# Kernel optimization log

Hardware: AMD Instinct MI355X
Metric: run time of the kernel (lower is better)

The kernel has to match this reference:

```python
import jax, jax.numpy as jnp
import numpy as np

N_NODES = 100000
N_EDGES = 1600000
D_IN, D_HID, D_OUT = 256, 256, 128


def setup_inputs() -> dict:
    key = jax.random.key(0)
    k1, k2, k3, k4, k5, k6 = jax.random.split(key, 6)
    x = jax.random.normal(k1, (N_NODES, D_IN), dtype=jnp.float32)
    edge_index = jax.random.randint(k2, (2, N_EDGES), 0, N_NODES, dtype=jnp.int64)
    W1 = jax.random.normal(k3, (D_IN, D_HID), dtype=jnp.float32) / np.sqrt(D_IN)
    b1 = jax.random.normal(k4, (D_HID,), dtype=jnp.float32) * 0.01
    W2 = jax.random.normal(k5, (D_HID, D_OUT), dtype=jnp.float32) / np.sqrt(D_HID)
    b2 = jax.random.normal(k6, (D_OUT,), dtype=jnp.float32) * 0.01
    return {"x": x, "edge_index": edge_index, "W1": W1, "b1": b1, "W2": W2, "b2": b2}


def _gcn_conv(x, src, dst, W, b, n_nodes):
    # PyG GCNConv: linear transform, add self-loops, symmetric normalization,
    # scatter-add aggregation, bias.
    h = x @ W                                         # [N, D_out]
    # degree including self-loop (edge weight 1)
    deg = jax.ops.segment_sum(jnp.ones((src.shape[0],), h.dtype), dst,
                              num_segments=n_nodes) + 1.0
    dinv = jax.lax.rsqrt(deg)                         # [N]
    norm = dinv[src] * dinv[dst]                      # [E]
    msg = h[src] * norm[:, None]                      # [E, D_out] gather + scale
    agg = jax.ops.segment_sum(msg, dst, num_segments=n_nodes)
    # self-loop contribution: norm_ii = dinv_i^2
    agg = agg + h * (dinv * dinv)[:, None]
    return agg + b


def reference(x, edge_index, W1, b1, W2, b2):
    src, dst = edge_index[0], edge_index[1]
    n = x.shape[0]
    h = _gcn_conv(x, src, dst, W1, b1, n)
    h = jax.nn.relu(h)
    out = _gcn_conv(h, src, dst, W2, b2, n)
    return out
```

## Files before the change

kernel.cpp:

```cpp
#include <hip/hip_runtime.h>

#define N_NODES 100000
#define N_EDGES 1600000
#define D_IN 256
#define D_HID 256
#define D_OUT 128
#define SLOTS 64

#define NB 1024
#define NPB 98
#define CAP 2048
#define BIN_T 8192

typedef unsigned int u32;
typedef unsigned short u16;
typedef __attribute__((ext_vector_type(8))) short bf16x8;
typedef __attribute__((ext_vector_type(8))) unsigned short u16x8;
typedef __attribute__((ext_vector_type(4))) float f32x4;

__device__ __forceinline__ u16 f2bf(float v) {
    u32 u = __float_as_uint(v);
    u32 r = (u + 0x7fffu + ((u >> 16) & 1u)) >> 16;
    return (u16)r;
}
__device__ __forceinline__ float bf2f(u16 b) {
    return __uint_as_float(((u32)b) << 16);
}

__global__ __launch_bounds__(256) void bin_kernel(const int* __restrict__ src,
                                                  const int* __restrict__ dst,
                                                  int* __restrict__ gcnt,
                                                  int* __restrict__ binned, int E,
                                                  const float* __restrict__ W1,
                                                  u16* __restrict__ w1hi,
                                                  const float* __restrict__ W2,
                                                  u16* __restrict__ w2hi) {
    const int t = threadIdx.x;
    const int gtid = blockIdx.x * 256 + t;
    const int gstride = gridDim.x * 256;
    for (int i = gtid; i < D_IN * D_HID; i += gstride) {
        const int k = i / D_HID, n = i - k * D_HID;
        w1hi[(size_t)n * D_IN + k] = f2bf(W1[i]);
    }
    for (int i = gtid; i < D_HID * D_OUT; i += gstride) {
        const int k = i / D_OUT, n = i - k * D_OUT;
        w2hi[(size_t)n * D_HID + k] = f2bf(W2[i]);
    }

    __shared__ int hist[NB];
    __shared__ int cur[NB];
    const int base = blockIdx.x * BIN_T;
#pragma unroll
    for (int q = 0; q < NB / 256; ++q) hist[q * 256 + t] = 0;
    __syncthreads();
#pragma unroll 4
    for (int j = 0; j < BIN_T / 256; ++j) {
        const int e = base + j * 256 + t;
        if (e < E) atomicAdd(&hist[dst[e] / NPB], 1);
    }
    __syncthreads();
#pragma unroll
    for (int q = 0; q < NB / 256; ++q) {
        const int b = q * 256 + t;
        const int c = hist[b];
        cur[b] = c ? atomicAdd(&gcnt[b], c) : 0;
    }
    __syncthreads();
#pragma unroll 4
    for (int j = 0; j < BIN_T / 256; ++j) {
        const int e = base + j * 256 + t;
        if (e < E) {
            const int d = dst[e];
            const int b = d / NPB;
            const int ld = d - b * NPB;
            const int r = atomicAdd(&cur[b], 1);
            if (r < CAP) binned[(size_t)b * CAP + r] = (ld << 17) | src[e];
        }
    }
}

__global__ __launch_bounds__(256) void bucket_scatter(const int* __restrict__ gcnt,
                                                      const int* __restrict__ binned,
                                                      int* __restrict__ deg,
                                                      int* __restrict__ slot,
                                                      float* __restrict__ dinv) {
    __shared__ int degw[NPB];
    __shared__ int slotw[NPB * SLOTS];
    const int b = blockIdx.x;
    const int t = threadIdx.x;
    const int nbase = b * NPB;
    for (int i = t; i < NPB; i += 256) degw[i] = 0;
    __syncthreads();
    int cnt = gcnt[b];
    if (cnt > CAP) cnt = CAP;
    const int* ep = &binned[(size_t)b * CAP];
    for (int i = t; i < cnt; i += 256) {
        const int v = ep[i];
        const int ld = v >> 17;
        const int s = v & 0x1FFFF;
        const int pos = atomicAdd(&degw[ld], 1);
        if (pos < SLOTS) slotw[ld * SLOTS + pos] = s;
    }
    __syncthreads();
    const int lim = min(NPB, N_NODES - nbase);
    if (lim <= 0) return;
    for (int i = t; i < lim * SLOTS; i += 256)
        slot[(size_t)nbase * SLOTS + i] = slotw[i];
    for (int i = t; i < lim; i += 256) {
        const int dgv = degw[i];
        deg[nbase + i] = dgv;
        dinv[nbase + i] = rsqrtf((float)dgv + 1.0f);
    }
}

template <bool AF32>
__global__ __launch_bounds__(256) void gemm_tile(
    const void* __restrict__ Aptr, const u16* __restrict__ B,
    u16* __restrict__ Cb, int M, int N, int K) {
    constexpr int ABYTES = AF32 ? 16384 : 8192;
    __shared__ char lds[2][ABYTES + 8192];
    const int t = threadIdx.x;
    const int wave = t >> 6;
    const int lane = t & 63;
    const int wm = wave >> 1, wn = wave & 1;
    const int mBase = blockIdx.y * 128;
    const int nBase = blockIdx.x * 128;

    f32x4 acc[4][4];
#pragma unroll
    for (int i = 0; i < 4; ++i)
#pragma unroll
        for (int j = 0; j < 4; ++j) acc[i][j] = (f32x4){0.f, 0.f, 0.f, 0.f};

    const int lr = lane >> 3;
    const int lp = lane & 7;
    const int lc = lp ^ lr;
    const int lr4 = lane >> 2;
    const int lc4 = (lane & 3) ^ (lr4 & 3);

    auto STAGE = [&](int buf, int kt) {
        const int k0 = kt * 32;
        if (AF32) {
            const float* A = (const float*)Aptr;
            const int coff = k0 + lc * 4;
#pragma unroll
            for (int q = 0; q < 4; ++q) {
                const int row = wave * 32 + q * 8 + lr;
                int mg = mBase + row;
                if (mg > M - 1) mg = M - 1;
                const float* s = A + (size_t)mg * K + coff;
                char* d = &lds[buf][(wave * 32 + q * 8) * 128];
                __builtin_amdgcn_global_load_lds(
                    (const __attribute__((address_space(1))) u32*)s,
                    (__attribute__((address_space(3))) u32*)d, 16, 0, 0);
            }
        } else {
            const u16* A = (const u16*)Aptr;
            const int coff = k0 + lc4 * 8;
#pragma unroll
            for (int q = 0; q < 2; ++q) {
                const int row = wave * 32 + q * 16 + lr4;
                int mg = mBase + row;
                if (mg > M - 1) mg = M - 1;
                const u16* s = A + (size_t)mg * K + coff;
                char* d = &lds[buf][(wave * 32 + q * 16) * 64];
                __builtin_amdgcn_global_load_lds(
                    (const __attribute__((address_space(1))) u32*)s,
                    (__attribute__((address_space(3))) u32*)d, 16, 0, 0);
            }
        }
        {
            const int coff = k0 + lc4 * 8;
#pragma unroll
            for (int q = 0; q < 2; ++q) {
                const int row = wave * 32 + q * 16 + lr4;
                const int ng = nBase + row;
                const u16* s = B + (size_t)ng * K + coff;
                char* d = &lds[buf][ABYTES + (wave * 32 + q * 16) * 64];
                __builtin_amdgcn_global_load_lds(
                    (const __attribute__((address_space(1))) u32*)s,
                    (__attribute__((address_space(3))) u32*)d, 16, 0, 0);
            }
        }
    };

    auto COMPUTE = [&](int buf) {
        const char* pa = &lds[buf][0];
        const char* pb = &lds[buf][ABYTES];
        const int lm = lane & 15;
        const int c4 = lane >> 4;
        bf16x8 ah[4], bh[4];
#pragma unroll
        for (int i = 0; i < 4; ++i) {
            const int r = wm * 64 + i * 16 + lm;
            if (AF32) {
                const int s = r & 7;
                const f32x4 a0 = *(const f32x4*)(pa + r * 128 + ((2 * c4) ^ s) * 16);
                const f32x4 a1 = *(const f32x4*)(pa + r * 128 + ((2 * c4 + 1) ^ s) * 16);
                bf16x8 h;
#pragma unroll
                for (int j = 0; j < 4; ++j)
                    h[j] = (short)((__float_as_uint(a0[j]) + 0x8000u) >> 16);
#pragma unroll
                for (int j = 0; j < 4; ++j)
                    h[4 + j] = (short)((__float_as_uint(a1[j]) + 0x8000u) >> 16);
                ah[i] = h;
            } else {
                ah[i] = *(const bf16x8*)(pa + r * 64 + (c4 ^ (r & 3)) * 16);
            }
        }
#pragma unroll
        for (int j = 0; j < 4; ++j) {
            const int r = wn * 64 + j * 16 + lm;
            bh[j] = *(const bf16x8*)(pb + r * 64 + (c4 ^ (r & 3)) * 16);
        }
#pragma unroll
        for (int i = 0; i < 4; ++i)
#pragma unroll
            for (int j = 0; j < 4; ++j)
                acc[i][j] = __builtin_amdgcn_mfma_f32_16x16x32_bf16(ah[i], bh[j], acc[i][j], 0, 0, 0);
    };

    const int NT = K / 32;
    STAGE(0, 0);
#pragma unroll 1
    for (int kt = 0; kt < NT; ++kt) {
        __syncthreads();
        if (kt + 1 < NT) STAGE((kt + 1) & 1, kt + 1);
        COMPUTE(kt & 1);
        __syncthreads();
    }

    const int lm = lane & 15;
    const int c4 = lane >> 4;
#pragma unroll
    for (int i = 0; i < 4; ++i) {
#pragma unroll
        for (int r = 0; r < 4; ++r) {
            const int row = mBase + wm * 64 + i * 16 + c4 * 4 + r;
            if (row < M) {
#pragma unroll
                for (int j = 0; j < 4; ++j) {
                    const int col = nBase + wn * 64 + j * 16 + lm;
                    Cb[(size_t)row * N + col] = f2bf(acc[i][j][r]);
                }
            }
        }
    }
}

__global__ __launch_bounds__(256) void gather_agg_bf16(const u16* __restrict__ h,
                                                       const int* __restrict__ deg,
                                                       const int* __restrict__ slot,
                                                       const float* __restrict__ dinv,
                                                       const float* __restrict__ bias,
                                                       u16* __restrict__ ob, int n) {
    const int node = blockIdx.x * 8 + (threadIdx.x >> 5);
    const int lane = threadIdx.x & 31;
    if (node >= n) return;
    const float di = dinv[node];
    int dg = deg[node];
    if (dg > SLOTS) dg = SLOTS;
    const int* sp = &slot[(size_t)node * SLOTS];
    const int off = lane * 8;

    float acc[8];
#pragma unroll
    for (int j = 0; j < 8; ++j) acc[j] = 0.f;

    int k = 0;
    for (; k + 1 < dg; k += 2) {
        const int s0 = sp[k];
        const int s1 = sp[k + 1];
        const float n0 = dinv[s0] * di;
        const float n1 = dinv[s1] * di;
        const u16x8 va = *(const u16x8*)&h[(size_t)s0 * 256 + off];
        const u16x8 vb = *(const u16x8*)&h[(size_t)s1 * 256 + off];
#pragma unroll
        for (int j = 0; j < 8; ++j)
            acc[j] += bf2f(va[j]) * n0 + bf2f(vb[j]) * n1;
    }
    if (k < dg) {
        const int s0 = sp[k];
        const float n0 = dinv[s0] * di;
        const u16x8 va = *(const u16x8*)&h[(size_t)s0 * 256 + off];
#pragma unroll
        for (int j = 0; j < 8; ++j) acc[j] += bf2f(va[j]) * n0;
    }

    const float sl = di * di;
    const u16x8 hv = *(const u16x8*)&h[(size_t)node * 256 + off];
    const float4 bv0 = *(const float4*)&bias[off];
    const float4 bv1 = *(const float4*)&bias[off + 4];
    const float bb[8] = {bv0.x, bv0.y, bv0.z, bv0.w, bv1.x, bv1.y, bv1.z, bv1.w};
    u16x8 H;
#pragma unroll
    for (int j = 0; j < 8; ++j)
        H[j] = f2bf(fmaxf(acc[j] + bf2f(hv[j]) * sl + bb[j], 0.f));
    *(u16x8*)&ob[(size_t)node * 256 + off] = H;
}

__global__ __launch_bounds__(256) void gather_agg_out(const u16* __restrict__ h,
                                                      const int* __restrict__ deg,
                                                      const int* __restrict__ slot,
                                                      const float* __restrict__ dinv,
                                                      const float* __restrict__ bias,
                                                      float* __restrict__ outp, int n) {
    const int node = blockIdx.x * 16 + (threadIdx.x >> 4);
    const int lane = threadIdx.x & 15;
    if (node >= n) return;
    const float di = dinv[node];
    int dg = deg[node];
    if (dg > SLOTS) dg = SLOTS;
    const int* sp = &slot[(size_t)node * SLOTS];
    const int off = lane * 8;

    float acc[8];
#pragma unroll
    for (int j = 0; j < 8; ++j) acc[j] = 0.f;

    int k = 0;
    for (; k + 1 < dg; k += 2) {
        const int s0 = sp[k];
        const int s1 = sp[k + 1];
        const float n0 = dinv[s0] * di;
        const float n1 = dinv[s1] * di;
        const u16x8 va = *(const u16x8*)&h[(size_t)s0 * 128 + off];
        const u16x8 vb = *(const u16x8*)&h[(size_t)s1 * 128 + off];
#pragma unroll
        for (int j = 0; j < 8; ++j)
            acc[j] += bf2f(va[j]) * n0 + bf2f(vb[j]) * n1;
    }
    if (k < dg) {
        const int s0 = sp[k];
        const float n0 = dinv[s0] * di;
        const u16x8 va = *(const u16x8*)&h[(size_t)s0 * 128 + off];
#pragma unroll
        for (int j = 0; j < 8; ++j) acc[j] += bf2f(va[j]) * n0;
    }

    const float sl = di * di;
    const u16x8 hv = *(const u16x8*)&h[(size_t)node * 128 + off];
    const float4 bv0 = *(const float4*)&bias[off];
    const float4 bv1 = *(const float4*)&bias[off + 4];
    const float bb[8] = {bv0.x, bv0.y, bv0.z, bv0.w, bv1.x, bv1.y, bv1.z, bv1.w};
    float o[8];
#pragma unroll
    for (int j = 0; j < 8; ++j) o[j] = acc[j] + bf2f(hv[j]) * sl + bb[j];
    float4 o0 = make_float4(o[0], o[1], o[2], o[3]);
    float4 o1 = make_float4(o[4], o[5], o[6], o[7]);
    *(float4*)&outp[(size_t)node * 128 + off] = o0;
    *(float4*)&outp[(size_t)node * 128 + off + 4] = o1;
}

extern "C" void kernel_launch(void* const* d_in, const int* in_sizes, int n_in,
                              void* d_out, int out_size, void* d_ws, size_t ws_size,
                              hipStream_t stream) {
    const float* x  = (const float*)d_in[0];
    const int*   ei = (const int*)d_in[1];
    const float* W1 = (const float*)d_in[2];
    const float* b1 = (const float*)d_in[3];
    const float* W2 = (const float*)d_in[4];
    const float* b2 = (const float*)d_in[5];
    float* out = (float*)d_out;

    const int* src = ei;
    const int* dst = ei + N_EDGES;

    char* ws = (char*)d_ws;
    float* dinv = (float*)(ws + 0x000000);
    int*   deg  = (int*)  (ws + 0x080000);
    int*   gcnt = (int*)  (ws + 0x100000);
    u16* wt1hi = (u16*)(ws + 0x200000);
    u16* wt2hi = (u16*)(ws + 0x240000);
    int* binned = (int*)(ws + 0x280000);
    int* slot   = (int*)(ws + 0xB00000);
    const size_t big = 0x2500000;
    u16* Phi = (u16*)(ws + big);
    u16* Hb  = (u16*)(ws + big + 51200000);

    hipMemsetAsync(gcnt, 0, NB * sizeof(int), stream);

    bin_kernel<<<(N_EDGES + BIN_T - 1) / BIN_T, 256, 0, stream>>>(
        src, dst, gcnt, binned, N_EDGES, W1, wt1hi, W2, wt2hi);
    bucket_scatter<<<NB, 256, 0, stream>>>(gcnt, binned, deg, slot, dinv);

    {
        dim3 g(D_HID / 128, (N_NODES + 127) / 128);
        gemm_tile<true><<<g, 256, 0, stream>>>(x, wt1hi, Hb, N_NODES, D_HID, D_IN);
    }
    gather_agg_bf16<<<(N_NODES + 7) / 8, 256, 0, stream>>>(
        Hb, deg, slot, dinv, b1, Phi, N_NODES);

    {
        dim3 g(D_OUT / 128, (N_NODES + 127) / 128);
        gemm_tile<false><<<g, 256, 0, stream>>>(Phi, wt2hi, Hb, N_NODES, D_OUT, D_HID);
    }
    gather_agg_out<<<(N_NODES + 15) / 16, 256, 0, stream>>>(
        Hb, deg, slot, dinv, b2, out, N_NODES);
}
```

Measured before the change: 325.7 us.

## Fuse edge binning with first GEMM in one launch, move weight conversion out

```diff
diff --git a/kernel.cpp b/kernel.cpp
--- a/kernel.cpp
+++ b/kernel.cpp
@@ -11,6 +11,9 @@
 #define NPB 98
 #define CAP 2048
 #define BIN_T 8192
+#define BIN_BLKS ((N_EDGES + BIN_T - 1) / BIN_T)
+#define GEMM1_ROWTILES ((N_NODES + 127) / 128)
+#define GEMM1_BLKS (GEMM1_ROWTILES * 2)
 
 typedef unsigned int u32;
 typedef unsigned short u16;
@@ -27,17 +30,13 @@
     return __uint_as_float(((u32)b) << 16);
 }
 
-__global__ __launch_bounds__(256) void bin_kernel(const int* __restrict__ src,
-                                                  const int* __restrict__ dst,
-                                                  int* __restrict__ gcnt,
-                                                  int* __restrict__ binned, int E,
-                                                  const float* __restrict__ W1,
-                                                  u16* __restrict__ w1hi,
-                                                  const float* __restrict__ W2,
-                                                  u16* __restrict__ w2hi) {
-    const int t = threadIdx.x;
-    const int gtid = blockIdx.x * 256 + t;
+__global__ __launch_bounds__(256) void weights_kernel(
+    const float* __restrict__ W1, u16* __restrict__ w1hi,
+    const float* __restrict__ W2, u16* __restrict__ w2hi,
+    int* __restrict__ gcnt) {
+    const int gtid = blockIdx.x * 256 + threadIdx.x;
     const int gstride = gridDim.x * 256;
+    for (int i = gtid; i < NB; i += gstride) gcnt[i] = 0;
     for (int i = gtid; i < D_IN * D_HID; i += gstride) {
         const int k = i / D_HID, n = i - k * D_HID;
         w1hi[(size_t)n * D_IN + k] = f2bf(W1[i]);
@@ -46,35 +45,161 @@
         const int k = i / D_OUT, n = i - k * D_OUT;
         w2hi[(size_t)n * D_HID + k] = f2bf(W2[i]);
     }
-
-    __shared__ int hist[NB];
-    __shared__ int cur[NB];
-    const int base = blockIdx.x * BIN_T;
-#pragma unroll
-    for (int q = 0; q < NB / 256; ++q) hist[q * 256 + t] = 0;
-    __syncthreads();
+}
+
+__global__ __launch_bounds__(256) void fused_bin_gemm1(
+    const int* __restrict__ src, const int* __restrict__ dst,
+    int* __restrict__ gcnt, int* __restrict__ binned,
+    const float* __restrict__ x, const u16* __restrict__ B,
+    u16* __restrict__ Cb) {
+    __shared__ char smem[49152];
+    const int t = threadIdx.x;
+
+    if (blockIdx.x < BIN_BLKS) {
+        int* hist = (int*)smem;
+        int* cur = hist + NB;
+        const int base = blockIdx.x * BIN_T;
+#pragma unroll
+        for (int q = 0; q < NB / 256; ++q) hist[q * 256 + t] = 0;
+        __syncthreads();
 #pragma unroll 4
-    for (int j = 0; j < BIN_T / 256; ++j) {
-        const int e = base + j * 256 + t;
-        if (e < E) atomicAdd(&hist[dst[e] / NPB], 1);
-    }
-    __syncthreads();
-#pragma unroll
-    for (int q = 0; q < NB / 256; ++q) {
-        const int b = q * 256 + t;
-        const int c = hist[b];
-        cur[b] = c ? atomicAdd(&gcnt[b], c) : 0;
-    }
-    __syncthreads();
+        for (int j = 0; j < BIN_T / 256; ++j) {
+            const int e = base + j * 256 + t;
+            if (e < N_EDGES) atomicAdd(&hist[dst[e] / NPB], 1);
+        }
+        __syncthreads();
+#pragma unroll
+        for (int q = 0; q < NB / 256; ++q) {
+            const int b = q * 256 + t;
+            const int c = hist[b];
+            cur[b] = c ? atomicAdd(&gcnt[b], c) : 0;
+        }
+        __syncthreads();
 #pragma unroll 4
-    for (int j = 0; j < BIN_T / 256; ++j) {
-        const int e = base + j * 256 + t;
-        if (e < E) {
-            const int d = dst[e];
-            const int b = d / NPB;
-            const int ld = d - b * NPB;
-            const int r = atomicAdd(&cur[b], 1);
-            if (r < CAP) binned[(size_t)b * CAP + r] = (ld << 17) | src[e];
+        for (int j = 0; j < BIN_T / 256; ++j) {
+            const int e = base + j * 256 + t;
+            if (e < N_EDGES) {
+                const int d = dst[e];
+                const int b = d / NPB;
+                const int ld = d - b * NPB;
+                const int r = atomicAdd(&cur[b], 1);
+                if (r < CAP) binned[(size_t)b * CAP + r] = (ld << 17) | src[e];
+            }
+        }
+        return;
+    }
+
+    const int bid = blockIdx.x - BIN_BLKS;
+    const int mBase = (bid >> 1) * 128;
+    const int nBase = (bid & 1) * 128;
+    constexpr int ABYTES = 16384;
+    constexpr int BUF = ABYTES + 8192;
+    const int wave = t >> 6;
+    const int lane = t & 63;
+    const int wm = wave >> 1, wn = wave & 1;
+    const int K = D_IN, N = D_HID, M = N_NODES;
+
+    f32x4 acc[4][4];
+#pragma unroll
+    for (int i = 0; i < 4; ++i)
+#pragma unroll
+        for (int j = 0; j < 4; ++j) acc[i][j] = (f32x4){0.f, 0.f, 0.f, 0.f};
+
+    const int lr = lane >> 3;
+    const int lp = lane & 7;
+    const int lc = lp ^ lr;
+    const int lr4 = lane >> 2;
+    const int lc4 = (lane & 3) ^ (lr4 & 3);
+
+    auto STAGE = [&](int buf, int kt) {
+        const int k0 = kt * 32;
+        char* ldsbuf = smem + buf * BUF;
+        {
+            const int coff = k0 + lc * 4;
+#pragma unroll
+            for (int q = 0; q < 4; ++q) {
+                const int row = wave * 32 + q * 8 + lr;
+                int mg = mBase + row;
+                if (mg > M - 1) mg = M - 1;
+                const float* s = x + (size_t)mg * K + coff;
+                char* d = ldsbuf + (wave * 32 + q * 8) * 128;
+                __builtin_amdgcn_global_load_lds(
+                    (const __attribute__((address_space(1))) u32*)s,
+                    (__attribute__((address_space(3))) u32*)d, 16, 0, 0);
+            }
+        }
+        {
+            const int coff = k0 + lc4 * 8;
+#pragma unroll
+            for (int q = 0; q < 2; ++q) {
+                const int row = wave * 32 + q * 16 + lr4;
+                const int ng = nBase + row;
+                const u16* s = B + (size_t)ng * K + coff;
+                char* d = ldsbuf + ABYTES + (wave * 32 + q * 16) * 64;
+                __builtin_amdgcn_global_load_lds(
+                    (const __attribute__((address_space(1))) u32*)s,
+                    (__attribute__((address_space(3))) u32*)d, 16, 0, 0);
+            }
+        }
+    };
+
+    auto COMPUTE = [&](int buf) {
+        const char* pa = smem + buf * BUF;
+        const char* pb = pa + ABYTES;
+        const int lm = lane & 15;
+        const int c4 = lane >> 4;
+        bf16x8 ah[4], bh[4];
+#pragma unroll
+        for (int i = 0; i < 4; ++i) {
+            const int r = wm * 64 + i * 16 + lm;
+            const int s = r & 7;
+            const f32x4 a0 = *(const f32x4*)(pa + r * 128 + ((2 * c4) ^ s) * 16);
+            const f32x4 a1 = *(const f32x4*)(pa + r * 128 + ((2 * c4 + 1) ^ s) * 16);
+            bf16x8 h;
+#pragma unroll
+            for (int j = 0; j < 4; ++j)
+                h[j] = (short)((__float_as_uint(a0[j]) + 0x8000u) >> 16);
+#pragma unroll
+            for (int j = 0; j < 4; ++j)
+                h[4 + j] = (short)((__float_as_uint(a1[j]) + 0x8000u) >> 16);
+            ah[i] = h;
+        }
+#pragma unroll
+        for (int j = 0; j < 4; ++j) {
+            const int r = wn * 64 + j * 16 + lm;
+            bh[j] = *(const bf16x8*)(pb + r * 64 + (c4 ^ (r & 3)) * 16);
+        }
+#pragma unroll
+        for (int i = 0; i < 4; ++i)
+#pragma unroll
+            for (int j = 0; j < 4; ++j)
+                acc[i][j] = __builtin_amdgcn_mfma_f32_16x16x32_bf16(ah[i], bh[j], acc[i][j], 0, 0, 0);
+    };
+
+    const int NT = K / 32;
+    STAGE(0, 0);
+#pragma unroll 1
+    for (int kt = 0; kt < NT; ++kt) {
+        __syncthreads();
+        if (kt + 1 < NT) STAGE((kt + 1) & 1, kt + 1);
+        COMPUTE(kt & 1);
+        __syncthreads();
+    }
+
+    const int lm = lane & 15;
+    const int c4 = lane >> 4;
+#pragma unroll
+    for (int i = 0; i < 4; ++i) {
+#pragma unroll
+        for (int r = 0; r < 4; ++r) {
+            const int row = mBase + wm * 64 + i * 16 + c4 * 4 + r;
+            if (row < M) {
+#pragma unroll
+                for (int j = 0; j < 4; ++j) {
+                    const int col = nBase + wn * 64 + j * 16 + lm;
+                    Cb[(size_t)row * N + col] = f2bf(acc[i][j][r]);
+                }
+            }
         }
     }
 }
@@ -113,11 +238,10 @@
     }
 }
 
-template <bool AF32>
-__global__ __launch_bounds__(256) void gemm_tile(
-    const void* __restrict__ Aptr, const u16* __restrict__ B,
+__global__ __launch_bounds__(256) void gemm_bf16(
+    const u16* __restrict__ A, const u16* __restrict__ B,
     u16* __restrict__ Cb, int M, int N, int K) {
-    constexpr int ABYTES = AF32 ? 16384 : 8192;
+    constexpr int ABYTES = 8192;
     __shared__ char lds[2][ABYTES + 8192];
     const int t = threadIdx.x;
     const int wave = t >> 6;
@@ -132,55 +256,32 @@
 #pragma unroll
         for (int j = 0; j < 4; ++j) acc[i][j] = (f32x4){0.f, 0.f, 0.f, 0.f};
 
-    const int lr = lane >> 3;
-    const int lp = lane & 7;
-    const int lc = lp ^ lr;
     const int lr4 = lane >> 2;
     const int lc4 = (lane & 3) ^ (lr4 & 3);
 
     auto STAGE = [&](int buf, int kt) {
         const int k0 = kt * 32;
-        if (AF32) {
-            const float* A = (const float*)Aptr;
-            const int coff = k0 + lc * 4;
-#pragma unroll
-            for (int q = 0; q < 4; ++q) {
-                const int row = wave * 32 + q * 8 + lr;
-                int mg = mBase + row;
-                if (mg > M - 1) mg = M - 1;
-                const float* s = A + (size_t)mg * K + coff;
-                char* d = &lds[buf][(wave * 32 + q * 8) * 128];
-                __builtin_amdgcn_global_load_lds(
-                    (const __attribute__((address_space(1))) u32*)s,
-                    (__attribute__((address_space(3))) u32*)d, 16, 0, 0);
-            }
-        } else {
-            const u16* A = (const u16*)Aptr;
-            const int coff = k0 + lc4 * 8;
-#pragma unroll
-            for (int q = 0; q < 2; ++q) {
-                const int row = wave * 32 + q * 16 + lr4;
-                int mg = mBase + row;
-                if (mg > M - 1) mg = M - 1;
-                const u16* s = A + (size_t)mg * K + coff;
-                char* d = &lds[buf][(wave * 32 + q * 16) * 64];
-                __builtin_amdgcn_global_load_lds(
-                    (const __attribute__((address_space(1))) u32*)s,
-                    (__attribute__((address_space(3))) u32*)d, 16, 0, 0);
-            }
-        }
-        {
-            const int coff = k0 + lc4 * 8;
-#pragma unroll
-            for (int q = 0; q < 2; ++q) {
-                const int row = wave * 32 + q * 16 + lr4;
-                const int ng = nBase + row;
-                const u16* s = B + (size_t)ng * K + coff;
-                char* d = &lds[buf][ABYTES + (wave * 32 + q * 16) * 64];
-                __builtin_amdgcn_global_load_lds(
-                    (const __attribute__((address_space(1))) u32*)s,
-                    (__attribute__((address_space(3))) u32*)d, 16, 0, 0);
-            }
+        const int coff = k0 + lc4 * 8;
+#pragma unroll
+        for (int q = 0; q < 2; ++q) {
+            const int row = wave * 32 + q * 16 + lr4;
+            int mg = mBase + row;
+            if (mg > M - 1) mg = M - 1;
+            const u16* s = A + (size_t)mg * K + coff;
+            char* d = &lds[buf][(wave * 32 + q * 16) * 64];
+            __builtin_amdgcn_global_load_lds(
+                (const __attribute__((address_space(1))) u32*)s,
+                (__attribute__((address_space(3))) u32*)d, 16, 0, 0);
+        }
+#pragma unroll
+        for (int q = 0; q < 2; ++q) {
+            const int row = wave * 32 + q * 16 + lr4;
+            const int ng = nBase + row;
+            const u16* s = B + (size_t)ng * K + coff;
+            char* d = &lds[buf][ABYTES + (wave * 32 + q * 16) * 64];
+            __builtin_amdgcn_global_load_lds(
+                (const __attribute__((address_space(1))) u32*)s,
+                (__attribute__((address_space(3))) u32*)d, 16, 0, 0);
         }
     };
 
@@ -193,21 +294,7 @@
 #pragma unroll
         for (int i = 0; i < 4; ++i) {
             const int r = wm * 64 + i * 16 + lm;
-            if (AF32) {
-                const int s = r & 7;
-                const f32x4 a0 = *(const f32x4*)(pa + r * 128 + ((2 * c4) ^ s) * 16);
-                const f32x4 a1 = *(const f32x4*)(pa + r * 128 + ((2 * c4 + 1) ^ s) * 16);
-                bf16x8 h;
-#pragma unroll
-                for (int j = 0; j < 4; ++j)
-                    h[j] = (short)((__float_as_uint(a0[j]) + 0x8000u) >> 16);
-#pragma unroll
-                for (int j = 0; j < 4; ++j)
-                    h[4 + j] = (short)((__float_as_uint(a1[j]) + 0x8000u) >> 16);
-                ah[i] = h;
-            } else {
-                ah[i] = *(const bf16x8*)(pa + r * 64 + (c4 ^ (r & 3)) * 16);
-            }
+            ah[i] = *(const bf16x8*)(pa + r * 64 + (c4 ^ (r & 3)) * 16);
         }
 #pragma unroll
         for (int j = 0; j < 4; ++j) {
@@ -379,22 +466,19 @@
     u16* Phi = (u16*)(ws + big);
     u16* Hb  = (u16*)(ws + big + 51200000);
 
-    hipMemsetAsync(gcnt, 0, NB * sizeof(int), stream);
-
-    bin_kernel<<<(N_EDGES + BIN_T - 1) / BIN_T, 256, 0, stream>>>(
-        src, dst, gcnt, binned, N_EDGES, W1, wt1hi, W2, wt2hi);
+    weights_kernel<<<96, 256, 0, stream>>>(W1, wt1hi, W2, wt2hi, gcnt);
+
+    fused_bin_gemm1<<<BIN_BLKS + GEMM1_BLKS, 256, 0, stream>>>(
+        src, dst, gcnt, binned, x, wt1hi, Hb);
+
     bucket_scatter<<<NB, 256, 0, stream>>>(gcnt, binned, deg, slot, dinv);
 
-    {
-        dim3 g(D_HID / 128, (N_NODES + 127) / 128);
-        gemm_tile<true><<<g, 256, 0, stream>>>(x, wt1hi, Hb, N_NODES, D_HID, D_IN);
-    }
     gather_agg_bf16<<<(N_NODES + 7) / 8, 256, 0, stream>>>(
         Hb, deg, slot, dinv, b1, Phi, N_NODES);
 
     {
         dim3 g(D_OUT / 128, (N_NODES + 127) / 128);
-        gemm_tile<false><<<g, 256, 0, stream>>>(Phi, wt2hi, Hb, N_NODES, D_OUT, D_HID);
+        gemm_bf16<<<g, 256, 0, stream>>>(Phi, wt2hi, Hb, N_NODES, D_OUT, D_HID);
     }
     gather_agg_out<<<(N_NODES + 15) / 16, 256, 0, stream>>>(
         Hb, deg, slot, dinv, b2, out, N_NODES);
```

Result: faster. 303.5 us, median of 2 (-6.8%).
